# Performance work log

Hardware: AMD Instinct MI355X
Metric: run time of the kernel (lower is better)

Reference implementation:

```python
import jax, jax.numpy as jnp
import numpy as np

B, S, D, R = 2, 2048, 1024, 224  # batch, seq, n_embd, table_size


def setup_inputs() -> dict:
    key = jax.random.key(0)
    k = jax.random.split(key, 6)
    return {
        "hidden_states": jax.random.normal(k[0], (B, S, D), jnp.float32),
        "w_row": jax.random.normal(k[1], (D, R), jnp.float32) * 0.02,
        "b_row": jnp.zeros((R,), jnp.float32),
        "col_weight": jax.random.normal(k[2], (R, D, R), jnp.float32) * 0.02,
        "col_bias": jnp.zeros((R, R), jnp.float32),
        "target_row_ids": jax.random.randint(k[3], (B, S), 0, R, jnp.int32),
        "target_col_ids": jax.random.randint(k[4], (B, S), 0, R, jnp.int32),
    }


def reference(hidden_states, w_row, b_row, col_weight, col_bias,
              target_row_ids, target_col_ids):
    Bv, Sv, Dv = hidden_states.shape
    Rv = col_bias.shape[0]
    N = Bv * Sv
    hs_flat = hidden_states.reshape(N, Dv)
    r = target_row_ids.reshape(N)
    c = target_col_ids.reshape(N)

    # row loss: standard cross entropy over table_size row logits (mean)
    row_logits = hs_flat @ w_row + b_row                      # [N, R]
    logp_row = jax.nn.log_softmax(row_logits, axis=-1)
    loss_row = -jnp.take_along_axis(logp_row, r[:, None].astype(jnp.int32), axis=1)[:, 0].mean()

    # column loss: per-token row-routed projection + cross entropy (sum / N).
    # Mathematically identical to the original per-row masked loop: each token
    # uses col_weight[row_id] / col_bias[row_id]. We process tokens in fixed-size
    # chunks with lax.scan so FLOPs match the original (N*D*R, not N*R*D*R) and
    # the gathered per-token weights stay bounded in memory.
    CHUNK = 256  # N = 4096 divisible by CHUNK
    hs_c = hs_flat.reshape(N // CHUNK, CHUNK, Dv)
    r_c = r.reshape(N // CHUNK, CHUNK)
    c_c = c.reshape(N // CHUNK, CHUNK)

    def body(acc, xs):
        h, ri, ci = xs                          # [C,D], [C], [C]
        w = col_weight[ri]                      # [C, D, R] irregular gather
        b = col_bias[ri]                        # [C, R]
        logits = jnp.einsum('cd,cdk->ck', h, w) + b
        logp = jax.nn.log_softmax(logits, axis=-1)
        nll = -jnp.take_along_axis(logp, ci[:, None].astype(jnp.int32), axis=1)[:, 0]
        return acc + nll.sum(), None

    loss_col_sum, _ = jax.lax.scan(body, jnp.float32(0.0), (hs_c, r_c, c_c))
    loss_col = loss_col_sum / N
    return loss_row + loss_col
```

## Files before the change

### kernel.cpp

```cpp
#include <hip/hip_runtime.h>
#include <math.h>

#define D_DIM 1024
#define R_DIM 224
#define N_TOK 4096
#define KC 64
#define MT 128
#define NTHREADS 448
#define COL_BLOCKS R_DIM
#define ROW_BLOCKS (N_TOK / MT)
#define GRID (COL_BLOCKS + ROW_BLOCKS)

typedef short bf16x8 __attribute__((ext_vector_type(8)));
typedef short short8_t __attribute__((ext_vector_type(8)));
typedef float floatx4 __attribute__((ext_vector_type(4)));

__device__ __forceinline__ short f2bf(float f) {
    unsigned u = __float_as_uint(f);
    u += 0x7fffu + ((u >> 16) & 1u);
    return (short)(u >> 16);
}

__device__ __forceinline__ void lds_barrier() {
    asm volatile("s_waitcnt lgkmcnt(0)" ::: "memory");
    __builtin_amdgcn_s_barrier();
}

__global__ __launch_bounds__(1024) void sort_kernel(
    const int* __restrict__ rid, int* __restrict__ sorted,
    int* __restrict__ cnt, int* __restrict__ off, float* __restrict__ out)
{
    __shared__ int h[256];
    __shared__ int sc[2][256];
    __shared__ int cur[R_DIM];
    const int tid = threadIdx.x;
    if (tid < 256) h[tid] = 0;
    __syncthreads();
    for (int n = tid; n < N_TOK; n += 1024) atomicAdd(&h[rid[n]], 1);
    __syncthreads();
    if (tid < 256) sc[0][tid] = h[tid];
    __syncthreads();
    int src = 0;
    for (int d = 1; d < 256; d <<= 1) {
        if (tid < 256) {
            int v = sc[src][tid];
            if (tid >= d) v += sc[src][tid - d];
            sc[src ^ 1][tid] = v;
        }
        __syncthreads();
        src ^= 1;
    }
    if (tid < R_DIM) {
        int o = sc[src][tid] - h[tid];
        off[tid] = o;
        cnt[tid] = h[tid];
        cur[tid] = o;
    }
    if (tid == 0) out[0] = 0.0f;
    __syncthreads();
    for (int n = tid; n < N_TOK; n += 1024) {
        int p = atomicAdd(&cur[rid[n]], 1);
        sorted[p] = n;
    }
}

__global__ __launch_bounds__(NTHREADS) void fused_kernel(
    const float* __restrict__ hs, const float* __restrict__ w_row,
    const float* __restrict__ b_row, const float* __restrict__ w_col,
    const float* __restrict__ b_col, const int* __restrict__ rid,
    const int* __restrict__ cid, const int* __restrict__ sorted,
    const int* __restrict__ cnt, const int* __restrict__ off,
    float* __restrict__ out)
{
    __shared__ short A_sh[MT * KC];
    __shared__ float Log_sh[16 * R_DIM];
    __shared__ float bias_sh[R_DIM];
    __shared__ int   tok_sh[MT];
    __shared__ float blk_sum;

    const int bid = blockIdx.x;
    const int tid = threadIdx.x;
    const int lane = tid & 63;
    const int wv = tid >> 6;
    const int lm = lane & 15;
    const int lg = lane >> 4;

    const bool is_row = (bid >= COL_BLOCKS);
    const int rho = is_row ? 0 : bid;
    const int tokbase = is_row ? (bid - COL_BLOCKS) * MT : off[rho];
    const int n_tok  = is_row ? MT : cnt[rho];
    const float* W    = is_row ? w_row : (w_col + (size_t)rho * D_DIM * R_DIM);
    const float* bias = is_row ? b_row : (b_col + (size_t)rho * R_DIM);

    if (tid == 0) blk_sum = 0.0f;
    for (int i = tid; i < R_DIM; i += NTHREADS) bias_sh[i] = bias[i];

    char* const Abp = (char*)A_sh;

    const int n_chunks = (n_tok + MT - 1) / MT;
    for (int p = 0; p < n_chunks; ++p) {
        const int mlim   = min(MT, n_tok - p * MT);
        const int mtiles = (mlim + 15) >> 4;
        const int mrows  = mtiles << 4;

        lds_barrier();
        if (tid < MT) {
            int gi = p * MT + tid;
            tok_sh[tid] = (gi < n_tok)
                ? (is_row ? (tokbase + gi) : sorted[tokbase + gi]) : -1;
        }

        floatx4 acc[8][2];
#pragma unroll
        for (int ms = 0; ms < 8; ++ms)
#pragma unroll
            for (int nt = 0; nt < 2; ++nt) acc[ms][nt] = (floatx4)0.0f;

        for (int kc = 0; kc < D_DIM / KC; ++kc) {
            const int K0 = kc * KC;
            float braw[2][2][8];
#pragma unroll
            for (int ks = 0; ks < 2; ++ks)
#pragma unroll
                for (int nt = 0; nt < 2; ++nt) {
                    const float* bp = W + (size_t)(K0 + ks * 32 + lg * 8) * R_DIM
                                        + (wv * 32 + nt * 16 + lm);
#pragma unroll
                    for (int j = 0; j < 8; ++j) braw[ks][nt][j] = bp[j * R_DIM];
                }

            lds_barrier();
            for (int i = tid; i < mrows * (KC / 8); i += NTHREADS) {
                int row = i >> 3;
                int g8 = i & 7;
                int tok = tok_sh[row];
                float4 h0 = make_float4(0.f, 0.f, 0.f, 0.f);
                float4 h1 = make_float4(0.f, 0.f, 0.f, 0.f);
                if (tok >= 0) {
                    const float* hp = &hs[(size_t)tok * D_DIM + K0 + g8 * 8];
                    h0 = *reinterpret_cast<const float4*>(hp);
                    h1 = *reinterpret_cast<const float4*>(hp + 4);
                }
                short8_t v = { f2bf(h0.x), f2bf(h0.y), f2bf(h0.z), f2bf(h0.w),
                               f2bf(h1.x), f2bf(h1.y), f2bf(h1.z), f2bf(h1.w) };
                *reinterpret_cast<short8_t*>(
                    Abp + row * 128 + ((g8 * 16) ^ ((row & 7) << 4))) = v;
            }
            lds_barrier();

            bf16x8 bfrag[2][2];
#pragma unroll
            for (int ks = 0; ks < 2; ++ks)
#pragma unroll
                for (int nt = 0; nt < 2; ++nt) {
                    bf16x8 v = { f2bf(braw[ks][nt][0]), f2bf(braw[ks][nt][1]),
                                 f2bf(braw[ks][nt][2]), f2bf(braw[ks][nt][3]),
                                 f2bf(braw[ks][nt][4]), f2bf(braw[ks][nt][5]),
                                 f2bf(braw[ks][nt][6]), f2bf(braw[ks][nt][7]) };
                    bfrag[ks][nt] = v;
                }
#pragma unroll
            for (int ks = 0; ks < 2; ++ks) {
                const int kbyte = ks * 64 + lg * 16;
#pragma unroll
                for (int ms = 0; ms < 8; ++ms) {
                    if (ms < mtiles) {
                        int row = ms * 16 + lm;
                        bf16x8 a = *reinterpret_cast<const bf16x8*>(
                            Abp + row * 128 + (kbyte ^ ((row & 7) << 4)));
                        acc[ms][0] = __builtin_amdgcn_mfma_f32_16x16x32_bf16(
                            a, bfrag[ks][0], acc[ms][0], 0, 0, 0);
                        acc[ms][1] = __builtin_amdgcn_mfma_f32_16x16x32_bf16(
                            a, bfrag[ks][1], acc[ms][1], 0, 0, 0);
                    }
                }
            }
        }

#pragma unroll
        for (int ms = 0; ms < 8; ++ms) {
            if (ms < mtiles) {
                lds_barrier();
#pragma unroll
                for (int nt = 0; nt < 2; ++nt) {
                    int col = wv * 32 + nt * 16 + lm;
#pragma unroll
                    for (int r = 0; r < 4; ++r) {
                        Log_sh[(lg * 4 + r) * R_DIM + col] =
                            acc[ms][nt][r] + bias_sh[col];
                    }
                }
                lds_barrier();
                const int mv = mlim - ms * 16;
                for (int rep = 0; rep < 3; ++rep) {
                    int t = wv + rep * 7;
                    if (t < 16 && t < mv) {
                        float m = -1e30f;
                        for (int c = lane; c < R_DIM; c += 64)
                            m = fmaxf(m, Log_sh[t * R_DIM + c]);
#pragma unroll
                        for (int s = 32; s; s >>= 1) m = fmaxf(m, __shfl_xor(m, s));
                        float sum = 0.0f;
                        for (int c = lane; c < R_DIM; c += 64)
                            sum += __expf(Log_sh[t * R_DIM + c] - m);
#pragma unroll
                        for (int s = 32; s; s >>= 1) sum += __shfl_xor(sum, s);
                        if (lane == 0) {
                            int n = tok_sh[ms * 16 + t];
                            int tgt = is_row ? rid[n] : cid[n];
                            float nll = -(Log_sh[t * R_DIM + tgt] - m - __logf(sum));
                            atomicAdd(&blk_sum, nll);
                        }
                    }
                }
            }
        }
    }
    __syncthreads();
    if (tid == 0) atomicAdd(out, blk_sum * (1.0f / N_TOK));
}

extern "C" void kernel_launch(void* const* d_in, const int* in_sizes, int n_in,
                              void* d_out, int out_size, void* d_ws, size_t ws_size,
                              hipStream_t stream)
{
    const float* hs    = (const float*)d_in[0];
    const float* w_row = (const float*)d_in[1];
    const float* b_row = (const float*)d_in[2];
    const float* w_col = (const float*)d_in[3];
    const float* b_col = (const float*)d_in[4];
    const int* rid     = (const int*)d_in[5];
    const int* cid     = (const int*)d_in[6];
    float* out = (float*)d_out;

    int* sorted = (int*)d_ws;
    int* cnt    = sorted + N_TOK;
    int* off    = cnt + R_DIM;

    hipLaunchKernelGGL(sort_kernel, dim3(1), dim3(1024), 0, stream,
                       rid, sorted, cnt, off, out);
    hipLaunchKernelGGL(fused_kernel, dim3(GRID), dim3(NTHREADS), 0, stream,
                       hs, w_row, b_row, w_col, b_col, rid, cid, sorted, cnt, off, out);
}
```

Before: 342.1 us.

## Split-K the routed GEMMs with atomic logit accumulation and a separate loss kernel

Splits the reduction dimension into four parts and processes tokens in smaller 32-row chunks, so the grid grows from 256 to roughly 1400 blocks and load imbalance across the per-row weight blocks shrinks. Partial logits are accumulated into global buffers with float atomics. A third kernel then computes the row and column softmax cross-entropy losses. An init kernel zeroes the logit buffers, which adds extra global memory traffic, atomic contention, and kernel launches.

```diff
diff --git a/kernel.cpp b/kernel.cpp
--- a/kernel.cpp
+++ b/kernel.cpp
@@ -4,12 +4,15 @@
 #define D_DIM 1024
 #define R_DIM 224
 #define N_TOK 4096
-#define KC 64
-#define MT 128
+#define KSPLIT 4
+#define KRANGE (D_DIM / KSPLIT)
+#define MCHUNK 32
 #define NTHREADS 448
-#define COL_BLOCKS R_DIM
-#define ROW_BLOCKS (N_TOK / MT)
-#define GRID (COL_BLOCKS + ROW_BLOCKS)
+#define COL_GRID (R_DIM * KSPLIT)
+#define ROW_MBLK (N_TOK / MCHUNK)
+#define ROW_GRID (ROW_MBLK * KSPLIT)
+#define GRID2 (COL_GRID + ROW_GRID)
+#define L_FLOATS (N_TOK * R_DIM)
 
 typedef short bf16x8 __attribute__((ext_vector_type(8)));
 typedef short short8_t __attribute__((ext_vector_type(8)));
@@ -21,19 +24,23 @@
     return (short)(u >> 16);
 }
 
-__device__ __forceinline__ void lds_barrier() {
-    asm volatile("s_waitcnt lgkmcnt(0)" ::: "memory");
-    __builtin_amdgcn_s_barrier();
-}
-
-__global__ __launch_bounds__(1024) void sort_kernel(
+__global__ __launch_bounds__(1024) void init_kernel(
     const int* __restrict__ rid, int* __restrict__ sorted,
-    int* __restrict__ cnt, int* __restrict__ off, float* __restrict__ out)
-{
+    int* __restrict__ cnt, int* __restrict__ off,
+    float* __restrict__ Lbuf, float* __restrict__ out)
+{
+    const int tid = threadIdx.x;
+    if (blockIdx.x != 0) {
+        const int zb = blockIdx.x - 1;
+        float4* Lp = reinterpret_cast<float4*>(Lbuf);
+        const int base = zb * 7168;
+        for (int i = tid; i < 7168; i += 1024)
+            Lp[base + i] = make_float4(0.f, 0.f, 0.f, 0.f);
+        return;
+    }
     __shared__ int h[256];
     __shared__ int sc[2][256];
     __shared__ int cur[R_DIM];
-    const int tid = threadIdx.x;
     if (tid < 256) h[tid] = 0;
     __syncthreads();
     for (int n = tid; n < N_TOK; n += 1024) atomicAdd(&h[rid[n]], 1);
@@ -64,19 +71,14 @@
     }
 }
 
-__global__ __launch_bounds__(NTHREADS) void fused_kernel(
+__global__ __launch_bounds__(NTHREADS) void gemm_kernel(
     const float* __restrict__ hs, const float* __restrict__ w_row,
-    const float* __restrict__ b_row, const float* __restrict__ w_col,
-    const float* __restrict__ b_col, const int* __restrict__ rid,
-    const int* __restrict__ cid, const int* __restrict__ sorted,
+    const float* __restrict__ w_col, const int* __restrict__ sorted,
     const int* __restrict__ cnt, const int* __restrict__ off,
-    float* __restrict__ out)
-{
-    __shared__ short A_sh[MT * KC];
-    __shared__ float Log_sh[16 * R_DIM];
-    __shared__ float bias_sh[R_DIM];
-    __shared__ int   tok_sh[MT];
-    __shared__ float blk_sum;
+    float* __restrict__ Lrow, float* __restrict__ Lcol)
+{
+    __shared__ short A_sh[MCHUNK * KRANGE];
+    __shared__ int tok_sh[MCHUNK];
 
     const int bid = blockIdx.x;
     const int tid = threadIdx.x;
@@ -85,139 +87,138 @@
     const int lm = lane & 15;
     const int lg = lane >> 4;
 
-    const bool is_row = (bid >= COL_BLOCKS);
-    const int rho = is_row ? 0 : bid;
-    const int tokbase = is_row ? (bid - COL_BLOCKS) * MT : off[rho];
-    const int n_tok  = is_row ? MT : cnt[rho];
-    const float* W    = is_row ? w_row : (w_col + (size_t)rho * D_DIM * R_DIM);
-    const float* bias = is_row ? b_row : (b_col + (size_t)rho * R_DIM);
-
-    if (tid == 0) blk_sum = 0.0f;
-    for (int i = tid; i < R_DIM; i += NTHREADS) bias_sh[i] = bias[i];
-
+    const bool is_row = (bid >= COL_GRID);
+    int ksp, tokbase, n_tok;
+    const float* W;
+    float* Ldst;
+    if (is_row) {
+        int idx = bid - COL_GRID;
+        ksp = idx & 3;
+        tokbase = (idx >> 2) * MCHUNK;
+        n_tok = MCHUNK;
+        W = w_row;
+        Ldst = Lrow;
+    } else {
+        int rho = bid >> 2;
+        ksp = bid & 3;
+        tokbase = off[rho];
+        n_tok = cnt[rho];
+        W = w_col + (size_t)rho * D_DIM * R_DIM;
+        Ldst = Lcol;
+    }
+    const int K0 = ksp * KRANGE;
     char* const Abp = (char*)A_sh;
-
-    const int n_chunks = (n_tok + MT - 1) / MT;
+    const int col0 = wv * 32 + lm;
+
+    const int n_chunks = (n_tok + MCHUNK - 1) / MCHUNK;
     for (int p = 0; p < n_chunks; ++p) {
-        const int mlim   = min(MT, n_tok - p * MT);
-        const int mtiles = (mlim + 15) >> 4;
-        const int mrows  = mtiles << 4;
-
-        lds_barrier();
-        if (tid < MT) {
-            int gi = p * MT + tid;
+        __syncthreads();
+        if (tid < MCHUNK) {
+            int gi = p * MCHUNK + tid;
             tok_sh[tid] = (gi < n_tok)
                 ? (is_row ? (tokbase + gi) : sorted[tokbase + gi]) : -1;
         }
-
-        floatx4 acc[8][2];
-#pragma unroll
-        for (int ms = 0; ms < 8; ++ms)
+        __syncthreads();
+        for (int i = tid; i < MCHUNK * (KRANGE / 8); i += NTHREADS) {
+            int row = i >> 5;
+            int g8 = i & 31;
+            int tok = tok_sh[row];
+            float4 h0 = make_float4(0.f, 0.f, 0.f, 0.f);
+            float4 h1 = make_float4(0.f, 0.f, 0.f, 0.f);
+            if (tok >= 0) {
+                const float* hp = &hs[(size_t)tok * D_DIM + K0 + g8 * 8];
+                h0 = *reinterpret_cast<const float4*>(hp);
+                h1 = *reinterpret_cast<const float4*>(hp + 4);
+            }
+            short8_t v = { f2bf(h0.x), f2bf(h0.y), f2bf(h0.z), f2bf(h0.w),
+                           f2bf(h1.x), f2bf(h1.y), f2bf(h1.z), f2bf(h1.w) };
+            *reinterpret_cast<short8_t*>(
+                Abp + row * 512 + ((g8 * 16) ^ ((row & 7) << 4))) = v;
+        }
+        __syncthreads();
+
+        floatx4 acc[2][2];
+#pragma unroll
+        for (int ms = 0; ms < 2; ++ms)
 #pragma unroll
             for (int nt = 0; nt < 2; ++nt) acc[ms][nt] = (floatx4)0.0f;
 
-        for (int kc = 0; kc < D_DIM / KC; ++kc) {
-            const int K0 = kc * KC;
-            float braw[2][2][8];
-#pragma unroll
-            for (int ks = 0; ks < 2; ++ks)
-#pragma unroll
-                for (int nt = 0; nt < 2; ++nt) {
-                    const float* bp = W + (size_t)(K0 + ks * 32 + lg * 8) * R_DIM
-                                        + (wv * 32 + nt * 16 + lm);
-#pragma unroll
-                    for (int j = 0; j < 8; ++j) braw[ks][nt][j] = bp[j * R_DIM];
-                }
-
-            lds_barrier();
-            for (int i = tid; i < mrows * (KC / 8); i += NTHREADS) {
-                int row = i >> 3;
-                int g8 = i & 7;
-                int tok = tok_sh[row];
-                float4 h0 = make_float4(0.f, 0.f, 0.f, 0.f);
-                float4 h1 = make_float4(0.f, 0.f, 0.f, 0.f);
+        for (int ks = 0; ks < 8; ++ks) {
+            const float* bp = W + (size_t)(K0 + ks * 32 + lg * 8) * R_DIM + col0;
+            float braw0[8], braw1[8];
+#pragma unroll
+            for (int j = 0; j < 8; ++j) braw0[j] = bp[j * R_DIM];
+#pragma unroll
+            for (int j = 0; j < 8; ++j) braw1[j] = bp[j * R_DIM + 16];
+            bf16x8 bf0 = { f2bf(braw0[0]), f2bf(braw0[1]), f2bf(braw0[2]), f2bf(braw0[3]),
+                           f2bf(braw0[4]), f2bf(braw0[5]), f2bf(braw0[6]), f2bf(braw0[7]) };
+            bf16x8 bf1 = { f2bf(braw1[0]), f2bf(braw1[1]), f2bf(braw1[2]), f2bf(braw1[3]),
+                           f2bf(braw1[4]), f2bf(braw1[5]), f2bf(braw1[6]), f2bf(braw1[7]) };
+            const int kbyte = ks * 64 + lg * 16;
+#pragma unroll
+            for (int ms = 0; ms < 2; ++ms) {
+                int row = ms * 16 + lm;
+                bf16x8 a = *reinterpret_cast<const bf16x8*>(
+                    Abp + row * 512 + (kbyte ^ ((row & 7) << 4)));
+                acc[ms][0] = __builtin_amdgcn_mfma_f32_16x16x32_bf16(a, bf0, acc[ms][0], 0, 0, 0);
+                acc[ms][1] = __builtin_amdgcn_mfma_f32_16x16x32_bf16(a, bf1, acc[ms][1], 0, 0, 0);
+            }
+        }
+
+#pragma unroll
+        for (int ms = 0; ms < 2; ++ms)
+#pragma unroll
+            for (int r = 0; r < 4; ++r) {
+                int mloc = ms * 16 + lg * 4 + r;
+                int tok = tok_sh[mloc];
                 if (tok >= 0) {
-                    const float* hp = &hs[(size_t)tok * D_DIM + K0 + g8 * 8];
-                    h0 = *reinterpret_cast<const float4*>(hp);
-                    h1 = *reinterpret_cast<const float4*>(hp + 4);
-                }
-                short8_t v = { f2bf(h0.x), f2bf(h0.y), f2bf(h0.z), f2bf(h0.w),
-                               f2bf(h1.x), f2bf(h1.y), f2bf(h1.z), f2bf(h1.w) };
-                *reinterpret_cast<short8_t*>(
-                    Abp + row * 128 + ((g8 * 16) ^ ((row & 7) << 4))) = v;
-            }
-            lds_barrier();
-
-            bf16x8 bfrag[2][2];
-#pragma unroll
-            for (int ks = 0; ks < 2; ++ks)
-#pragma unroll
-                for (int nt = 0; nt < 2; ++nt) {
-                    bf16x8 v = { f2bf(braw[ks][nt][0]), f2bf(braw[ks][nt][1]),
-                                 f2bf(braw[ks][nt][2]), f2bf(braw[ks][nt][3]),
-                                 f2bf(braw[ks][nt][4]), f2bf(braw[ks][nt][5]),
-                                 f2bf(braw[ks][nt][6]), f2bf(braw[ks][nt][7]) };
-                    bfrag[ks][nt] = v;
-                }
-#pragma unroll
-            for (int ks = 0; ks < 2; ++ks) {
-                const int kbyte = ks * 64 + lg * 16;
-#pragma unroll
-                for (int ms = 0; ms < 8; ++ms) {
-                    if (ms < mtiles) {
-                        int row = ms * 16 + lm;
-                        bf16x8 a = *reinterpret_cast<const bf16x8*>(
-                            Abp + row * 128 + (kbyte ^ ((row & 7) << 4)));
-                        acc[ms][0] = __builtin_amdgcn_mfma_f32_16x16x32_bf16(
-                            a, bfrag[ks][0], acc[ms][0], 0, 0, 0);
-                        acc[ms][1] = __builtin_amdgcn_mfma_f32_16x16x32_bf16(
-                            a, bfrag[ks][1], acc[ms][1], 0, 0, 0);
-                    }
+                    atomicAdd(&Ldst[(size_t)tok * R_DIM + col0], acc[ms][0][r]);
+                    atomicAdd(&Ldst[(size_t)tok * R_DIM + col0 + 16], acc[ms][1][r]);
                 }
             }
-        }
-
-#pragma unroll
-        for (int ms = 0; ms < 8; ++ms) {
-            if (ms < mtiles) {
-                lds_barrier();
-#pragma unroll
-                for (int nt = 0; nt < 2; ++nt) {
-                    int col = wv * 32 + nt * 16 + lm;
-#pragma unroll
-                    for (int r = 0; r < 4; ++r) {
-                        Log_sh[(lg * 4 + r) * R_DIM + col] =
-                            acc[ms][nt][r] + bias_sh[col];
-                    }
-                }
-                lds_barrier();
-                const int mv = mlim - ms * 16;
-                for (int rep = 0; rep < 3; ++rep) {
-                    int t = wv + rep * 7;
-                    if (t < 16 && t < mv) {
-                        float m = -1e30f;
-                        for (int c = lane; c < R_DIM; c += 64)
-                            m = fmaxf(m, Log_sh[t * R_DIM + c]);
-#pragma unroll
-                        for (int s = 32; s; s >>= 1) m = fmaxf(m, __shfl_xor(m, s));
-                        float sum = 0.0f;
-                        for (int c = lane; c < R_DIM; c += 64)
-                            sum += __expf(Log_sh[t * R_DIM + c] - m);
-#pragma unroll
-                        for (int s = 32; s; s >>= 1) sum += __shfl_xor(sum, s);
-                        if (lane == 0) {
-                            int n = tok_sh[ms * 16 + t];
-                            int tgt = is_row ? rid[n] : cid[n];
-                            float nll = -(Log_sh[t * R_DIM + tgt] - m - __logf(sum));
-                            atomicAdd(&blk_sum, nll);
-                        }
-                    }
-                }
-            }
-        }
-    }
-    __syncthreads();
-    if (tid == 0) atomicAdd(out, blk_sum * (1.0f / N_TOK));
+    }
+}
+
+__global__ __launch_bounds__(256) void loss_kernel(
+    const float* __restrict__ Lrow, const float* __restrict__ Lcol,
+    const float* __restrict__ b_row, const float* __restrict__ b_col,
+    const int* __restrict__ rid, const int* __restrict__ cid,
+    float* __restrict__ out)
+{
+    __shared__ float wsum[4];
+    const int tid = threadIdx.x;
+    const int lane = tid & 63;
+    const int wv = tid >> 6;
+    const int gw = blockIdx.x * 4 + wv;
+    float accum = 0.0f;
+
+    for (int n = gw; n < N_TOK; n += 512) {
+        const int rt = rid[n];
+        const int ct = cid[n];
+#pragma unroll
+        for (int part = 0; part < 2; ++part) {
+            const float* Lp = (part == 0 ? Lrow : Lcol) + (size_t)n * R_DIM;
+            const float* bp = (part == 0) ? b_row : (b_col + (size_t)rt * R_DIM);
+            const int tgt = (part == 0) ? rt : ct;
+            float v0 = Lp[lane] + bp[lane];
+            float v1 = Lp[lane + 64] + bp[lane + 64];
+            float v2 = Lp[lane + 128] + bp[lane + 128];
+            float v3 = (lane < 32) ? (Lp[lane + 192] + bp[lane + 192]) : -1e30f;
+            float m = fmaxf(fmaxf(v0, v1), fmaxf(v2, v3));
+#pragma unroll
+            for (int s = 32; s; s >>= 1) m = fmaxf(m, __shfl_xor(m, s));
+            float sum = __expf(v0 - m) + __expf(v1 - m) + __expf(v2 - m)
+                      + ((lane < 32) ? __expf(v3 - m) : 0.0f);
+#pragma unroll
+            for (int s = 32; s; s >>= 1) sum += __shfl_xor(sum, s);
+            float tl = Lp[tgt] + bp[tgt];
+            accum += -(tl - m - __logf(sum));
+        }
+    }
+    if (lane == 0) wsum[wv] = accum;
+    __syncthreads();
+    if (tid == 0)
+        atomicAdd(out, (wsum[0] + wsum[1] + wsum[2] + wsum[3]) * (1.0f / N_TOK));
 }
 
 extern "C" void kernel_launch(void* const* d_in, const int* in_sizes, int n_in,
@@ -233,12 +234,16 @@
     const int* cid     = (const int*)d_in[6];
     float* out = (float*)d_out;
 
-    int* sorted = (int*)d_ws;
+    float* Lrow = (float*)d_ws;
+    float* Lcol = Lrow + L_FLOATS;
+    int* sorted = (int*)(Lcol + L_FLOATS);
     int* cnt    = sorted + N_TOK;
     int* off    = cnt + R_DIM;
 
-    hipLaunchKernelGGL(sort_kernel, dim3(1), dim3(1024), 0, stream,
-                       rid, sorted, cnt, off, out);
-    hipLaunchKernelGGL(fused_kernel, dim3(GRID), dim3(NTHREADS), 0, stream,
-                       hs, w_row, b_row, w_col, b_col, rid, cid, sorted, cnt, off, out);
-}
+    hipLaunchKernelGGL(init_kernel, dim3(65), dim3(1024), 0, stream,
+                       rid, sorted, cnt, off, Lrow, out);
+    hipLaunchKernelGGL(gemm_kernel, dim3(GRID2), dim3(NTHREADS), 0, stream,
+                       hs, w_row, w_col, sorted, cnt, off, Lrow, Lcol);
+    hipLaunchKernelGGL(loss_kernel, dim3(128), dim3(256), 0, stream,
+                       Lrow, Lcol, b_row, b_col, rid, cid, out);
+}
```

Measured after the change: 338.4 us. No clear change (-1.1%).
